# Optimization experiments

Measured on AMD Instinct MI355X. Metric: run time of the kernel, lower is better.

The kernel has to match this reference:

```python
import jax, jax.numpy as jnp
import numpy as np

LAYERS = 20
STACKS = 2
LPS = LAYERS // STACKS  # layers per stack -> dilations 2**(l % LPS)
OUT_CH = 256
RES_CH = 64
GATE_CH = 128
SKIP_CH = 256


def setup_inputs() -> dict:
    key = jax.random.key(0)
    ks = jax.random.split(key, 16)
    B, T = 8, 16000
    s = 0.05
    inp = {
        "x": jax.random.normal(ks[0], (B, OUT_CH, T), dtype=jnp.float32),
        # first causal conv (note: original code applies w_pre to the shifted
        # input twice -> output is 2*w_pre(pre); w_cur is unused, so omitted)
        "w_pre0": jax.random.normal(ks[1], (RES_CH, OUT_CH)) * s,
        "b_pre0": jax.random.normal(ks[2], (RES_CH,)) * s,
        # per-layer dilated conv (no bias), residual block, skip projection
        "w_dil_pre": jax.random.normal(ks[3], (LAYERS, GATE_CH, RES_CH)) * s,
        "w_dil_cur": jax.random.normal(ks[4], (LAYERS, GATE_CH, RES_CH)) * s,
        "bias_h": jax.random.normal(ks[5], (LAYERS, GATE_CH)) * s,
        "w_res": jax.random.normal(ks[6], (LAYERS, RES_CH, RES_CH)) * s,
        "b_res": jax.random.normal(ks[7], (LAYERS, RES_CH)) * s,
        "w_skip": jax.random.normal(ks[8], (LAYERS, SKIP_CH, RES_CH)) * s,
        "b_skip": jax.random.normal(ks[9], (LAYERS, SKIP_CH)) * s,
        # output head
        "w_relu": jax.random.normal(ks[10], (SKIP_CH, SKIP_CH)) * s,
        "b_relu": jax.random.normal(ks[11], (SKIP_CH,)) * s,
        "w_out": jax.random.normal(ks[12], (OUT_CH, SKIP_CH)) * s,
        "b_out": jax.random.normal(ks[13], (OUT_CH,)) * s,
    }
    return inp


def _shift_right(h, d):
    # causal shift: pad d zeros on the left along time, drop last d samples
    return jnp.pad(h, ((0, 0), (0, 0), (d, 0)))[:, :, :-d]


def reference(x, w_pre0, b_pre0, w_dil_pre, w_dil_cur, bias_h,
              w_res, b_res, w_skip, b_skip, w_relu, b_relu, w_out, b_out):
    # first causal conv: original Conv2X1 'casual' path computes
    # w_pre(pre) + w_pre(pre) = 2 * w_pre(pre)  (faithful to source)
    pre = _shift_right(x, 1)
    h = 2.0 * (jnp.einsum('rc,bct->brt', w_pre0, pre) + b_pre0[None, :, None])

    skip = jnp.zeros((x.shape[0], SKIP_CH, x.shape[2]), dtype=h.dtype)
    for l in range(LAYERS):
        d = 2 ** (l % LPS)
        h_pre = _shift_right(h, d)
        # dilated 2x1 conv = two channel-wise linears (no bias), summed with bias_h
        a = (jnp.einsum('gr,brt->bgt', w_dil_pre[l], h_pre)
             + jnp.einsum('gr,brt->bgt', w_dil_cur[l], h)
             + bias_h[l][None, :, None])
        g = jnp.tanh(a[:, :RES_CH]) * jax.nn.sigmoid(a[:, RES_CH:])
        res = jnp.einsum('rq,bqt->brt', w_res[l], g) + b_res[l][None, :, None]
        h = h + res
        skip = skip + jnp.einsum('sr,brt->bst', w_skip[l], g) + b_skip[l][None, :, None]

    o = jax.nn.relu(skip)
    o = jnp.einsum('ps,bst->bpt', w_relu, o) + b_relu[None, :, None]
    o = jax.nn.relu(o)
    logits = jnp.einsum('os,bst->bot', w_out, o) + b_out[None, :, None]
    return jax.nn.softmax(logits, axis=1)  # (B, out_channels, T)
```

## Files before the change

kernel.cpp:

```cpp
#include <hip/hip_runtime.h>
#include <math.h>

#define B_ 8
#define T_ 16000
#define NBT 250
#define HROWS 16512
#define NLAY 20

typedef __attribute__((ext_vector_type(8))) short bf16x8;
typedef __attribute__((ext_vector_type(4))) float f32x4;
typedef __attribute__((ext_vector_type(4))) short sh4;

__device__ __forceinline__ unsigned short f2bf(float f){
  unsigned u = __float_as_uint(f);
  u += 0x7fffu + ((u >> 16) & 1u);
  return (unsigned short)(u >> 16);
}
__device__ __forceinline__ float bf2f(unsigned short s){
  return __uint_as_float(((unsigned)s) << 16);
}
__device__ __forceinline__ void split2(float v, unsigned short& hi, unsigned short& lo){
  hi = f2bf(v);
  lo = f2bf(v - bf2f(hi));
}

#define MFMA(a,b,c) __builtin_amdgcn_mfma_f32_16x16x32_bf16((a),(b),(c),0,0,0)

__device__ __forceinline__ void gload16(const short* gsrc, short* ldst){
  __builtin_amdgcn_global_load_lds(
      (const __attribute__((address_space(1))) unsigned int*)gsrc,
      (__attribute__((address_space(3))) unsigned int*)ldst, 16, 0, 0);
}

__global__ void k_split(const float* __restrict__ src, short* __restrict__ hi,
                        short* __restrict__ lo, int n){
  int idx = blockIdx.x * 256 + threadIdx.x;
  if (idx < n){
    unsigned short h, l; split2(src[idx], h, l);
    hi[idx] = (short)h; lo[idx] = (short)l;
  }
}
__global__ void k_split_hi(const float* __restrict__ src, short* __restrict__ hi, int n){
  int idx = blockIdx.x * 256 + threadIdx.x;
  if (idx < n) hi[idx] = (short)f2bf(src[idx]);
}
__global__ void k_split_gate(const float* __restrict__ wdp, const float* __restrict__ wdc,
                             short* __restrict__ hi, short* __restrict__ lo){
  int idx = blockIdx.x * 256 + threadIdx.x;
  if (idx < NLAY*128*128){
    int l   = idx >> 14;
    int rem = idx & 16383;
    int row = rem >> 7;
    int k   = rem & 127;
    float v = (k < 64) ? wdp[(l*128 + row)*64 + k] : wdc[(l*128 + row)*64 + (k-64)];
    unsigned short h, lo16; split2(v, h, lo16);
    hi[idx] = (short)h; lo[idx] = (short)lo16;
  }
}
__global__ void k_bsum(const float* __restrict__ bsk, float* __restrict__ bsum){
  int s = threadIdx.x;
  if (s < 256){
    float a = 0.f;
#pragma unroll
    for (int l = 0; l < NLAY; ++l) a += bsk[l*256 + s];
    bsum[s] = a;
  }
}
__global__ void k_zero_guard(short* __restrict__ hA, short* __restrict__ hB){
  int idx = blockIdx.x * 256 + threadIdx.x;
  if (idx < B_*512*128){
    int b = idx / (512*128);
    int rem = idx - b*(512*128);
    size_t off = (size_t)b*HROWS*128 + rem;
    hA[off] = 0; hB[off] = 0;
  }
}

__global__ __launch_bounds__(512) void k_head_in(
    const float* __restrict__ x, const short* __restrict__ wph,
    const short* __restrict__ wpl, const float* __restrict__ bias,
    short* __restrict__ h)
{
  __shared__ short SXh[64*256], SXl[64*256];
  const int tid = threadIdx.x;
  const int bb = blockIdx.x / NBT;
  const int t0 = (blockIdx.x % NBT) * 64;
  const int lane = tid & 63, w = tid >> 6;
  const int l16 = lane & 15, l4 = lane >> 4;

  const float* xb = x + (size_t)bb * 256 * T_;
  {
    int col = lane;
    int t = t0 + col - 1;
#pragma unroll
    for (int p = 0; p < 16; ++p){
      int k0 = w*32 + p*2;
      float v0 = (t >= 0) ? xb[(size_t)k0*T_ + t] : 0.f;
      float v1 = (t >= 0) ? xb[(size_t)(k0+1)*T_ + t] : 0.f;
      unsigned short h0,l0,h1,l1; split2(v0,h0,l0); split2(v1,h1,l1);
      int idx = col*256 + (k0 ^ ((col & 15) << 3));
      ((unsigned int*)SXh)[idx>>1] = (unsigned)h0 | ((unsigned)h1 << 16);
      ((unsigned int*)SXl)[idx>>1] = (unsigned)l0 | ((unsigned)l1 << 16);
    }
  }
  __syncthreads();

  const int mi = w & 3, nh = w >> 2;
  const int rowA = mi*16 + l16;
  const int rt0 = mi*16 + l4*4;
  bf16x8 Ah[8], Al[8];
#pragma unroll
  for (int kb = 0; kb < 8; ++kb){
    int ko = kb*32 + l4*8;
    Ah[kb] = *(const bf16x8*)(wph + (size_t)rowA*256 + ko);
    Al[kb] = *(const bf16x8*)(wpl + (size_t)rowA*256 + ko);
  }
  short* hb = h + ((size_t)bb*HROWS + 512)*128;
#pragma unroll
  for (int nt = 0; nt < 2; ++nt){
    int col = (nh*2 + nt)*16 + l16;
    f32x4 acc = {0.f,0.f,0.f,0.f};
#pragma unroll
    for (int kb = 0; kb < 8; ++kb){
      int ko = (kb*32 + l4*8) ^ (l16 << 3);
      bf16x8 bhv = *(const bf16x8*)&SXh[col*256 + ko];
      bf16x8 blv = *(const bf16x8*)&SXl[col*256 + ko];
      acc = MFMA(Ah[kb], bhv, acc);
      acc = MFMA(Ah[kb], blv, acc);
      acc = MFMA(Al[kb], bhv, acc);
    }
    int t = t0 + col;
    int key = t & 15;
    int c  = rt0 >> 3, sub = rt0 & 7;
    sh4 hv, lv;
#pragma unroll
    for (int r = 0; r < 4; ++r){
      float v = 2.f*(acc[r] + bias[rt0 + r]);
      unsigned short hh, ll; split2(v, hh, ll);
      hv[r] = (short)hh; lv[r] = (short)ll;
    }
    *(sh4*)&hb[(size_t)t*128 + ((c ^ key) << 3) + sub] = hv;
    *(sh4*)&hb[(size_t)t*128 + (((c + 8) ^ key) << 3) + sub] = lv;
  }
}

__global__ __launch_bounds__(512) void k_layer2(
    const short* __restrict__ hin, short* __restrict__ hout,
    short* __restrict__ gout,
    const short* __restrict__ wgh, const short* __restrict__ wgl,
    const short* __restrict__ wrh, const short* __restrict__ wrlo,
    const float* __restrict__ bh, const float* __restrict__ br, int d)
{
  __shared__ short SH[64*128];
  __shared__ short SHP[64*128];
  __shared__ short SGh[64*64], SGl[64*64];
  const int tid = threadIdx.x;
  const int bb = blockIdx.x / NBT;
  const int t0 = (blockIdx.x % NBT) * 64;
  const int lane = tid & 63, w = tid >> 6;
  const int l16 = lane & 15, l4 = lane >> 4;

  const short* hb = hin + ((size_t)bb*HROWS + 512)*128;
  {
#pragma unroll
    for (int i = 0; i < 2; ++i){
      int colb = (w*2 + i)*4;
      const short* s1 = hb + (size_t)(t0 + colb + (lane>>4))*128 + (lane&15)*8;
      gload16(s1, &SH[colb*128]);
      const short* s2 = hb + (size_t)(t0 - d + colb + (lane>>4))*128 + (lane&15)*8;
      gload16(s2, &SHP[colb*128]);
    }
  }

  const int mi = w & 3, nh = w >> 2;
  const int rt0 = mi*16 + l4*4;
  const int rowt = mi*16 + l16, rows = 64 + mi*16 + l16;
  bf16x8 Ath[4], Atl[4], Ash[4], Asl[4];
#pragma unroll
  for (int kb = 0; kb < 4; ++kb){
    int ko = kb*32 + l4*8;
    Ath[kb] = *(const bf16x8*)(wgh + (size_t)rowt*128 + ko);
    Atl[kb] = *(const bf16x8*)(wgl + (size_t)rowt*128 + ko);
    Ash[kb] = *(const bf16x8*)(wgh + (size_t)rows*128 + ko);
    Asl[kb] = *(const bf16x8*)(wgl + (size_t)rows*128 + ko);
  }
  float bt[4], bs[4];
#pragma unroll
  for (int r = 0; r < 4; ++r){ bt[r] = bh[rt0+r]; bs[r] = bh[64+rt0+r]; }
  __syncthreads();

#pragma unroll
  for (int nt = 0; nt < 2; ++nt){
    int col = (nh*2 + nt)*16 + l16;
    int keyC = col & 15;
    int keyP = (col - d) & 15;
    f32x4 at = {0.f,0.f,0.f,0.f}, as = {0.f,0.f,0.f,0.f};
#pragma unroll
    for (int kb = 0; kb < 4; ++kb){
      const short* tile = (kb < 2) ? SHP : SH;
      int key = (kb < 2) ? keyP : keyC;
      int cb = (kb & 1)*4 + l4;
      bf16x8 bhv = *(const bf16x8*)&tile[col*128 + ((cb ^ key) << 3)];
      bf16x8 blv = *(const bf16x8*)&tile[col*128 + (((cb + 8) ^ key) << 3)];
      at = MFMA(Ath[kb], bhv, at);
      at = MFMA(Ath[kb], blv, at);
      at = MFMA(Atl[kb], bhv, at);
      as = MFMA(Ash[kb], bhv, as);
      as = MFMA(Ash[kb], blv, as);
      as = MFMA(Asl[kb], bhv, as);
    }
    unsigned short gh4[4], gl4[4];
#pragma unroll
    for (int r = 0; r < 4; ++r){
      float av = at[r] + bt[r];
      float sv = as[r] + bs[r];
      float e2 = __expf(2.f*av);
      float tv = 1.f - 2.f/(e2 + 1.f);
      float sg = 1.f/(1.f + __expf(-sv));
      float g  = tv*sg;
      split2(g, gh4[r], gl4[r]);
      int gi = col*64 + ((rt0 + r) ^ ((col & 7) << 3));
      SGh[gi] = (short)gh4[r]; SGl[gi] = (short)gl4[r];
    }
    {
      int t = t0 + col;
      sh4 gv; gv[0]=(short)gh4[0]; gv[1]=(short)gh4[1]; gv[2]=(short)gh4[2]; gv[3]=(short)gh4[3];
      *(sh4*)(gout + ((size_t)bb*T_ + t)*64 + rt0) = gv;
    }
  }
  __syncthreads();

  {
    const int rowA = mi*16 + l16;
    bf16x8 Rh[2], Rl[2];
#pragma unroll
    for (int kb = 0; kb < 2; ++kb){
      int ko = kb*32 + l4*8;
      Rh[kb] = *(const bf16x8*)(wrh  + (size_t)rowA*64 + ko);
      Rl[kb] = *(const bf16x8*)(wrlo + (size_t)rowA*64 + ko);
    }
    short* ho = hout + ((size_t)bb*HROWS + 512)*128;
    const int cH = rt0 >> 3, sub = rt0 & 7;
#pragma unroll
    for (int nt = 0; nt < 2; ++nt){
      int col = (nh*2 + nt)*16 + l16;
      int keyC = col & 15;
      f32x4 acc = {0.f,0.f,0.f,0.f};
#pragma unroll
      for (int kb = 0; kb < 2; ++kb){
        int ko = (kb*32 + l4*8) ^ ((col & 7) << 3);
        bf16x8 bhv = *(const bf16x8*)&SGh[col*64 + ko];
        bf16x8 blv = *(const bf16x8*)&SGl[col*64 + ko];
        acc = MFMA(Rh[kb], bhv, acc);
        acc = MFMA(Rh[kb], blv, acc);
        acc = MFMA(Rl[kb], bhv, acc);
      }
      sh4 hi4 = *(const sh4*)&SH[col*128 + ((cH ^ keyC) << 3) + sub];
      sh4 lo4 = *(const sh4*)&SH[col*128 + (((cH + 8) ^ keyC) << 3) + sub];
      int t = t0 + col;
      sh4 hv, lv;
#pragma unroll
      for (int r = 0; r < 4; ++r){
        float hin_f = bf2f((unsigned short)hi4[r]) + bf2f((unsigned short)lo4[r]);
        float v = hin_f + acc[r] + br[rt0 + r];
        unsigned short hh, ll; split2(v, hh, ll);
        hv[r] = (short)hh; lv[r] = (short)ll;
      }
      *(sh4*)&ho[(size_t)t*128 + ((cH ^ keyC) << 3) + sub] = hv;
      *(sh4*)&ho[(size_t)t*128 + (((cH + 8) ^ keyC) << 3) + sub] = lv;
    }
  }
}

__global__ __launch_bounds__(512) void k_head_fused(
    float* __restrict__ io,
    const short* __restrict__ g,
    const short* __restrict__ wsk,
    const float* __restrict__ bsum,
    const short* __restrict__ wrlh, const short* __restrict__ wrll,
    const float* __restrict__ brl,
    const short* __restrict__ woh, const short* __restrict__ wol,
    const float* __restrict__ bo)
{
  __shared__ short GT[2][64*64];
  __shared__ short S1h[64*256];
  __shared__ float smax[8][64], ssum[8][64];
  const int tid = threadIdx.x;
  const int bb = blockIdx.x / NBT;
  const int t0 = (blockIdx.x % NBT) * 64;
  const int lane = tid & 63, w = tid >> 6;
  const int l16 = lane & 15, l4 = lane >> 4;

  const int r0 = w*32 + l16, r1 = w*32 + 16 + l16;
  const int rtb0 = w*32 + l4*4, rtb1 = rtb0 + 16;

  f32x4 acc0[4], acc1[4];
#pragma unroll
  for (int nt = 0; nt < 4; ++nt){ acc0[nt] = (f32x4){0.f,0.f,0.f,0.f}; acc1[nt] = (f32x4){0.f,0.f,0.f,0.f}; }

  const int str = w*8 + (lane >> 3);
  const int sc  = lane & 7;
  const size_t gsrc_off = ((size_t)bb*T_ + t0 + str)*64 + ((sc ^ (str & 7)) << 3);

#define STAGE(l20, buf) gload16(g + (size_t)(l20)*B_*T_*64 + gsrc_off, &GT[buf][w*512])

  STAGE(0, 0);
  __syncthreads();
  for (int l20 = 0; l20 < 20; ++l20){
    if (l20 + 1 < 20) STAGE(l20 + 1, (l20 + 1) & 1);
    const short* wl = wsk + (size_t)l20*256*64;
    const short* gt = &GT[l20 & 1][0];
#pragma unroll
    for (int kb2 = 0; kb2 < 2; ++kb2){
      int koW = kb2*32 + l4*8;
      bf16x8 A0 = *(const bf16x8*)(wl + (size_t)r0*64 + koW);
      bf16x8 A1 = *(const bf16x8*)(wl + (size_t)r1*64 + koW);
      int cc = kb2*4 + l4;
#pragma unroll
      for (int nt = 0; nt < 4; ++nt){
        int rr = nt*16 + l16;
        bf16x8 Bv = *(const bf16x8*)&gt[rr*64 + ((cc ^ (rr & 7)) << 3)];
        acc0[nt] = MFMA(A0, Bv, acc0[nt]);
        acc1[nt] = MFMA(A1, Bv, acc1[nt]);
      }
    }
    __syncthreads();
  }
#undef STAGE

  {
    float bs0[4], bs1[4];
#pragma unroll
    for (int r = 0; r < 4; ++r){ bs0[r] = bsum[rtb0+r]; bs1[r] = bsum[rtb1+r]; }
#pragma unroll
    for (int nt = 0; nt < 4; ++nt){
      int c2 = nt*16 + l16;
      unsigned short h[4];
#pragma unroll
      for (int r = 0; r < 4; ++r)
        h[r] = f2bf(fmaxf(acc0[nt][r] + bs0[r], 0.f));
      int i0 = c2*256 + (rtb0 ^ (l16 << 3));
      ((unsigned int*)&S1h[i0])[0] = (unsigned)h[0] | ((unsigned)h[1] << 16);
      ((unsigned int*)&S1h[i0])[1] = (unsigned)h[2] | ((unsigned)h[3] << 16);
#pragma unroll
      for (int r = 0; r < 4; ++r)
        h[r] = f2bf(fmaxf(acc1[nt][r] + bs1[r], 0.f));
      int i1 = c2*256 + (rtb1 ^ (l16 << 3));
      ((unsigned int*)&S1h[i1])[0] = (unsigned)h[0] | ((unsigned)h[1] << 16);
      ((unsigned int*)&S1h[i1])[1] = (unsigned)h[2] | ((unsigned)h[3] << 16);
    }
  }
  __syncthreads();

#pragma unroll
  for (int nt = 0; nt < 4; ++nt){ acc0[nt] = (f32x4){0.f,0.f,0.f,0.f}; acc1[nt] = (f32x4){0.f,0.f,0.f,0.f}; }
#pragma unroll
  for (int kb = 0; kb < 8; ++kb){
    int ko = kb*32 + l4*8;
    bf16x8 A0h = *(const bf16x8*)(wrlh + (size_t)r0*256 + ko);
    bf16x8 A0l = *(const bf16x8*)(wrll + (size_t)r0*256 + ko);
    bf16x8 A1h = *(const bf16x8*)(wrlh + (size_t)r1*256 + ko);
    bf16x8 A1l = *(const bf16x8*)(wrll + (size_t)r1*256 + ko);
#pragma unroll
    for (int nt = 0; nt < 4; ++nt){
      int c2 = nt*16 + l16;
      int kos = ko ^ (l16 << 3);
      bf16x8 bhv = *(const bf16x8*)&S1h[c2*256 + kos];
      acc0[nt] = MFMA(A0h, bhv, acc0[nt]);
      acc0[nt] = MFMA(A0l, bhv, acc0[nt]);
      acc1[nt] = MFMA(A1h, bhv, acc1[nt]);
      acc1[nt] = MFMA(A1l, bhv, acc1[nt]);
    }
  }
  __syncthreads();
  {
    float br0[4], br1[4];
#pragma unroll
    for (int r = 0; r < 4; ++r){ br0[r] = brl[rtb0+r]; br1[r] = brl[rtb1+r]; }
#pragma unroll
    for (int nt = 0; nt < 4; ++nt){
      int c2 = nt*16 + l16;
      unsigned short h[4];
#pragma unroll
      for (int r = 0; r < 4; ++r)
        h[r] = f2bf(fmaxf(acc0[nt][r] + br0[r], 0.f));
      int i0 = c2*256 + (rtb0 ^ (l16 << 3));
      ((unsigned int*)&S1h[i0])[0] = (unsigned)h[0] | ((unsigned)h[1] << 16);
      ((unsigned int*)&S1h[i0])[1] = (unsigned)h[2] | ((unsigned)h[3] << 16);
#pragma unroll
      for (int r = 0; r < 4; ++r)
        h[r] = f2bf(fmaxf(acc1[nt][r] + br1[r], 0.f));
      int i1 = c2*256 + (rtb1 ^ (l16 << 3));
      ((unsigned int*)&S1h[i1])[0] = (unsigned)h[0] | ((unsigned)h[1] << 16);
      ((unsigned int*)&S1h[i1])[1] = (unsigned)h[2] | ((unsigned)h[3] << 16);
    }
  }
  __syncthreads();

#pragma unroll
  for (int nt = 0; nt < 4; ++nt){ acc0[nt] = (f32x4){0.f,0.f,0.f,0.f}; acc1[nt] = (f32x4){0.f,0.f,0.f,0.f}; }
#pragma unroll
  for (int kb = 0; kb < 8; ++kb){
    int ko = kb*32 + l4*8;
    bf16x8 A0h = *(const bf16x8*)(woh + (size_t)r0*256 + ko);
    bf16x8 A0l = *(const bf16x8*)(wol + (size_t)r0*256 + ko);
    bf16x8 A1h = *(const bf16x8*)(woh + (size_t)r1*256 + ko);
    bf16x8 A1l = *(const bf16x8*)(wol + (size_t)r1*256 + ko);
#pragma unroll
    for (int nt = 0; nt < 4; ++nt){
      int c2 = nt*16 + l16;
      int kos = ko ^ (l16 << 3);
      bf16x8 bhv = *(const bf16x8*)&S1h[c2*256 + kos];
      acc0[nt] = MFMA(A0h, bhv, acc0[nt]);
      acc0[nt] = MFMA(A0l, bhv, acc0[nt]);
      acc1[nt] = MFMA(A1h, bhv, acc1[nt]);
      acc1[nt] = MFMA(A1l, bhv, acc1[nt]);
    }
  }
  float* iob = io + (size_t)bb * 256 * T_;
  float bo0[4], bo1[4];
#pragma unroll
  for (int r = 0; r < 4; ++r){ bo0[r] = bo[rtb0+r]; bo1[r] = bo[rtb1+r]; }
#pragma unroll
  for (int nt = 0; nt < 4; ++nt){
    float m = -1e30f;
#pragma unroll
    for (int r = 0; r < 4; ++r){
      acc0[nt][r] += bo0[r];
      acc1[nt][r] += bo1[r];
      m = fmaxf(m, fmaxf(acc0[nt][r], acc1[nt][r]));
    }
    m = fmaxf(m, __shfl_xor(m, 16, 64));
    m = fmaxf(m, __shfl_xor(m, 32, 64));
    smax[w][nt*16 + l16] = m;
  }
  __syncthreads();
#pragma unroll
  for (int nt = 0; nt < 4; ++nt){
    float m = smax[0][nt*16 + l16];
#pragma unroll
    for (int ww = 1; ww < 8; ++ww) m = fmaxf(m, smax[ww][nt*16 + l16]);
    float s = 0.f;
#pragma unroll
    for (int r = 0; r < 4; ++r){
      acc0[nt][r] = __expf(acc0[nt][r] - m); s += acc0[nt][r];
      acc1[nt][r] = __expf(acc1[nt][r] - m); s += acc1[nt][r];
    }
    s += __shfl_xor(s, 16, 64);
    s += __shfl_xor(s, 32, 64);
    ssum[w][nt*16 + l16] = s;
  }
  __syncthreads();
#pragma unroll
  for (int nt = 0; nt < 4; ++nt){
    float S = 0.f;
#pragma unroll
    for (int ww = 0; ww < 8; ++ww) S += ssum[ww][nt*16 + l16];
    float inv = 1.f / S;
    int t = t0 + nt*16 + l16;
#pragma unroll
    for (int r = 0; r < 4; ++r){
      iob[(size_t)(rtb0 + r)*T_ + t] = acc0[nt][r]*inv;
      iob[(size_t)(rtb1 + r)*T_ + t] = acc1[nt][r]*inv;
    }
  }
}

extern "C" void kernel_launch(void* const* d_in, const int* in_sizes, int n_in,
                              void* d_out, int out_size, void* d_ws, size_t ws_size,
                              hipStream_t stream) {
  const float* x       = (const float*)d_in[0];
  const float* w_pre0  = (const float*)d_in[1];
  const float* b_pre0  = (const float*)d_in[2];
  const float* w_dil_p = (const float*)d_in[3];
  const float* w_dil_c = (const float*)d_in[4];
  const float* bias_h  = (const float*)d_in[5];
  const float* w_res   = (const float*)d_in[6];
  const float* b_res   = (const float*)d_in[7];
  const float* w_skip  = (const float*)d_in[8];
  const float* b_skip  = (const float*)d_in[9];
  const float* w_relu  = (const float*)d_in[10];
  const float* b_relu  = (const float*)d_in[11];
  const float* w_out   = (const float*)d_in[12];
  const float* b_out   = (const float*)d_in[13];

  float* out = (float*)d_out;
  short* hA = (short*)d_ws;
  short* hB = hA + (size_t)B_ * HROWS * 128;
  float* bsum = (float*)(hB + (size_t)B_ * HROWS * 128);
  short* p   = (short*)(bsum + 256);
  short* WPh = p; p += 16384;  short* WPl = p; p += 16384;
  short* WGh = p; p += 327680; short* WGl = p; p += 327680;
  short* WRh = p; p += 81920;  short* WRl = p; p += 81920;
  short* WSh = p; p += 327680;
  short* WLh = p; p += 65536;  short* WLl = p; p += 65536;
  short* WOh = p; p += 65536;  short* WOl = p; p += 65536;
  short* GBUF = p;

  k_split<<<64, 256, 0, stream>>>(w_pre0, WPh, WPl, 16384);
  k_split_gate<<<1280, 256, 0, stream>>>(w_dil_p, w_dil_c, WGh, WGl);
  k_split<<<320, 256, 0, stream>>>(w_res, WRh, WRl, 81920);
  k_split_hi<<<1280, 256, 0, stream>>>(w_skip, WSh, 327680);
  k_split<<<256, 256, 0, stream>>>(w_relu, WLh, WLl, 65536);
  k_split<<<256, 256, 0, stream>>>(w_out, WOh, WOl, 65536);
  k_zero_guard<<<2048, 256, 0, stream>>>(hA, hB);
  k_bsum<<<1, 256, 0, stream>>>(b_skip, bsum);

  k_head_in<<<B_ * NBT, 512, 0, stream>>>(x, WPh, WPl, b_pre0, hA);

  const short* hin = hA;
  short* houtp = hB;
  for (int l = 0; l < NLAY; ++l) {
    int d = 1 << (l % 10);
    k_layer2<<<B_ * NBT, 512, 0, stream>>>(
        hin, houtp,
        GBUF + (size_t)l * B_ * T_ * 64,
        WGh + (size_t)l*16384, WGl + (size_t)l*16384,
        WRh + (size_t)l*4096,  WRl + (size_t)l*4096,
        bias_h + (size_t)l*128, b_res + (size_t)l*64, d);
    const short* tmp = hin;
    hin = houtp;
    houtp = (short*)tmp;
  }

  k_head_fused<<<B_ * NBT, 512, 0, stream>>>(
      out, GBUF, WSh, bsum, WLh, WLl, b_relu, WOh, WOl, b_out);
}
```

Before: 1.418 ms.

## Store gate activations and skip weights in MFMA fragment order for direct register loads

```diff
diff --git a/kernel.cpp b/kernel.cpp
--- a/kernel.cpp
+++ b/kernel.cpp
@@ -39,10 +39,6 @@
     unsigned short h, l; split2(src[idx], h, l);
     hi[idx] = (short)h; lo[idx] = (short)l;
   }
-}
-__global__ void k_split_hi(const float* __restrict__ src, short* __restrict__ hi, int n){
-  int idx = blockIdx.x * 256 + threadIdx.x;
-  if (idx < n) hi[idx] = (short)f2bf(src[idx]);
 }
 __global__ void k_split_gate(const float* __restrict__ wdp, const float* __restrict__ wdc,
                              short* __restrict__ hi, short* __restrict__ lo){
@@ -57,6 +53,20 @@
     hi[idx] = (short)h; lo[idx] = (short)lo16;
   }
 }
+__global__ void k_pack_wsf(const float* __restrict__ wsk, short* __restrict__ wsf){
+  int idx = blockIdx.x * 256 + threadIdx.x;
+  if (idx < NLAY*8*2*2*64*8){
+    int e    = idx & 7;
+    int j    = (idx >> 3) & 63;
+    int kb2  = (idx >> 9) & 1;
+    int half = (idx >> 10) & 1;
+    int w    = (idx >> 11) & 7;
+    int l    = idx >> 14;
+    int row  = w*32 + half*16 + (j & 15);
+    int ch   = (kb2*4 + (j >> 4))*8 + e;
+    wsf[idx] = (short)f2bf(wsk[((size_t)l*256 + row)*64 + ch]);
+  }
+}
 __global__ void k_bsum(const float* __restrict__ bsk, float* __restrict__ bsum){
   int s = threadIdx.x;
   if (s < 256){
@@ -144,7 +154,7 @@
   }
 }
 
-__global__ __launch_bounds__(512) void k_layer2(
+__global__ __launch_bounds__(512) void k_layer4(
     const short* __restrict__ hin, short* __restrict__ hout,
     short* __restrict__ gout,
     const short* __restrict__ wgh, const short* __restrict__ wgl,
@@ -156,7 +166,8 @@
   __shared__ short SGh[64*64], SGl[64*64];
   const int tid = threadIdx.x;
   const int bb = blockIdx.x / NBT;
-  const int t0 = (blockIdx.x % NBT) * 64;
+  const int tile = blockIdx.x % NBT;
+  const int t0 = tile * 64;
   const int lane = tid & 63, w = tid >> 6;
   const int l16 = lane & 15, l4 = lane >> 4;
 
@@ -197,11 +208,11 @@
     f32x4 at = {0.f,0.f,0.f,0.f}, as = {0.f,0.f,0.f,0.f};
 #pragma unroll
     for (int kb = 0; kb < 4; ++kb){
-      const short* tile = (kb < 2) ? SHP : SH;
+      const short* tile_p = (kb < 2) ? SHP : SH;
       int key = (kb < 2) ? keyP : keyC;
       int cb = (kb & 1)*4 + l4;
-      bf16x8 bhv = *(const bf16x8*)&tile[col*128 + ((cb ^ key) << 3)];
-      bf16x8 blv = *(const bf16x8*)&tile[col*128 + (((cb + 8) ^ key) << 3)];
+      bf16x8 bhv = *(const bf16x8*)&tile_p[col*128 + ((cb ^ key) << 3)];
+      bf16x8 blv = *(const bf16x8*)&tile_p[col*128 + (((cb + 8) ^ key) << 3)];
       at = MFMA(Ath[kb], bhv, at);
       at = MFMA(Ath[kb], blv, at);
       at = MFMA(Atl[kb], bhv, at);
@@ -222,13 +233,16 @@
       int gi = col*64 + ((rt0 + r) ^ ((col & 7) << 3));
       SGh[gi] = (short)gh4[r]; SGl[gi] = (short)gl4[r];
     }
-    {
-      int t = t0 + col;
-      sh4 gv; gv[0]=(short)gh4[0]; gv[1]=(short)gh4[1]; gv[2]=(short)gh4[2]; gv[3]=(short)gh4[3];
-      *(sh4*)(gout + ((size_t)bb*T_ + t)*64 + rt0) = gv;
-    }
-  }
-  __syncthreads();
+  }
+  __syncthreads();
+
+  {
+    int f = tid >> 6, j = tid & 63;
+    int row = (f >> 1)*16 + (j & 15);
+    int c   = (f & 1)*4 + (j >> 4);
+    bf16x8 v = *(const bf16x8*)&SGh[row*64 + ((c ^ (row & 7)) << 3)];
+    *(bf16x8*)(gout + ((size_t)bb*NBT + tile)*4096 + tid*8) = v;
+  }
 
   {
     const int rowA = mi*16 + l16;
@@ -275,19 +289,19 @@
 __global__ __launch_bounds__(512) void k_head_fused(
     float* __restrict__ io,
     const short* __restrict__ g,
-    const short* __restrict__ wsk,
+    const short* __restrict__ wsf,
     const float* __restrict__ bsum,
     const short* __restrict__ wrlh, const short* __restrict__ wrll,
     const float* __restrict__ brl,
     const short* __restrict__ woh, const short* __restrict__ wol,
     const float* __restrict__ bo)
 {
-  __shared__ short GT[2][64*64];
   __shared__ short S1h[64*256];
   __shared__ float smax[8][64], ssum[8][64];
   const int tid = threadIdx.x;
   const int bb = blockIdx.x / NBT;
-  const int t0 = (blockIdx.x % NBT) * 64;
+  const int tile = blockIdx.x % NBT;
+  const int t0 = tile * 64;
   const int lane = tid & 63, w = tid >> 6;
   const int l16 = lane & 15, l4 = lane >> 4;
 
@@ -298,35 +312,33 @@
 #pragma unroll
   for (int nt = 0; nt < 4; ++nt){ acc0[nt] = (f32x4){0.f,0.f,0.f,0.f}; acc1[nt] = (f32x4){0.f,0.f,0.f,0.f}; }
 
-  const int str = w*8 + (lane >> 3);
-  const int sc  = lane & 7;
-  const size_t gsrc_off = ((size_t)bb*T_ + t0 + str)*64 + ((sc ^ (str & 7)) << 3);
-
-#define STAGE(l20, buf) gload16(g + (size_t)(l20)*B_*T_*64 + gsrc_off, &GT[buf][w*512])
-
-  STAGE(0, 0);
-  __syncthreads();
-  for (int l20 = 0; l20 < 20; ++l20){
-    if (l20 + 1 < 20) STAGE(l20 + 1, (l20 + 1) & 1);
-    const short* wl = wsk + (size_t)l20*256*64;
-    const short* gt = &GT[l20 & 1][0];
-#pragma unroll
-    for (int kb2 = 0; kb2 < 2; ++kb2){
-      int koW = kb2*32 + l4*8;
-      bf16x8 A0 = *(const bf16x8*)(wl + (size_t)r0*64 + koW);
-      bf16x8 A1 = *(const bf16x8*)(wl + (size_t)r1*64 + koW);
-      int cc = kb2*4 + l4;
+  {
+    const size_t LSTR = (size_t)B_ * NBT * 4096;
+    const short* gb = g + ((size_t)bb*NBT + tile)*4096 + lane*8;
+    const short* wb = wsf + (size_t)w*2048 + lane*8;
+    for (int l20 = 0; l20 < 20; ++l20){
+      const short* gt = gb + (size_t)l20*LSTR;
+      const short* wl = wb + (size_t)l20*16384;
+      bf16x8 A00 = *(const bf16x8*)(wl);
+      bf16x8 A01 = *(const bf16x8*)(wl + 512);
+      bf16x8 A10 = *(const bf16x8*)(wl + 1024);
+      bf16x8 A11 = *(const bf16x8*)(wl + 1536);
+      bf16x8 Bv[4][2];
 #pragma unroll
       for (int nt = 0; nt < 4; ++nt){
-        int rr = nt*16 + l16;
-        bf16x8 Bv = *(const bf16x8*)&gt[rr*64 + ((cc ^ (rr & 7)) << 3)];
-        acc0[nt] = MFMA(A0, Bv, acc0[nt]);
-        acc1[nt] = MFMA(A1, Bv, acc1[nt]);
+#pragma unroll
+        for (int kb2 = 0; kb2 < 2; ++kb2)
+          Bv[nt][kb2] = *(const bf16x8*)(gt + (nt*2 + kb2)*512);
       }
-    }
-    __syncthreads();
-  }
-#undef STAGE
+#pragma unroll
+      for (int nt = 0; nt < 4; ++nt){
+        acc0[nt] = MFMA(A00, Bv[nt][0], acc0[nt]);
+        acc0[nt] = MFMA(A01, Bv[nt][1], acc0[nt]);
+        acc1[nt] = MFMA(A10, Bv[nt][0], acc1[nt]);
+        acc1[nt] = MFMA(A11, Bv[nt][1], acc1[nt]);
+      }
+    }
+  }
 
   {
     float bs0[4], bs1[4];
@@ -492,7 +504,7 @@
   short* WPh = p; p += 16384;  short* WPl = p; p += 16384;
   short* WGh = p; p += 327680; short* WGl = p; p += 327680;
   short* WRh = p; p += 81920;  short* WRl = p; p += 81920;
-  short* WSh = p; p += 327680;
+  short* WSF = p; p += 327680;
   short* WLh = p; p += 65536;  short* WLl = p; p += 65536;
   short* WOh = p; p += 65536;  short* WOl = p; p += 65536;
   short* GBUF = p;
@@ -500,7 +512,7 @@
   k_split<<<64, 256, 0, stream>>>(w_pre0, WPh, WPl, 16384);
   k_split_gate<<<1280, 256, 0, stream>>>(w_dil_p, w_dil_c, WGh, WGl);
   k_split<<<320, 256, 0, stream>>>(w_res, WRh, WRl, 81920);
-  k_split_hi<<<1280, 256, 0, stream>>>(w_skip, WSh, 327680);
+  k_pack_wsf<<<1280, 256, 0, stream>>>(w_skip, WSF);
   k_split<<<256, 256, 0, stream>>>(w_relu, WLh, WLl, 65536);
   k_split<<<256, 256, 0, stream>>>(w_out, WOh, WOl, 65536);
   k_zero_guard<<<2048, 256, 0, stream>>>(hA, hB);
@@ -512,9 +524,9 @@
   short* houtp = hB;
   for (int l = 0; l < NLAY; ++l) {
     int d = 1 << (l % 10);
-    k_layer2<<<B_ * NBT, 512, 0, stream>>>(
+    k_layer4<<<B_ * NBT, 512, 0, stream>>>(
         hin, houtp,
-        GBUF + (size_t)l * B_ * T_ * 64,
+        GBUF + (size_t)l * B_ * NBT * 4096,
         WGh + (size_t)l*16384, WGl + (size_t)l*16384,
         WRh + (size_t)l*4096,  WRl + (size_t)l*4096,
         bias_h + (size_t)l*128, b_res + (size_t)l*64, d);
@@ -524,5 +536,5 @@
   }
 
   k_head_fused<<<B_ * NBT, 512, 0, stream>>>(
-      out, GBUF, WSh, bsum, WLh, WLl, b_relu, WOh, WOl, b_out);
-}
+      out, GBUF, WSF, bsum, WLh, WLl, b_relu, WOh, WOl, b_out);
+}
```

Result: slower. 1.468 ms (+3.5%).
